# Kernel optimization log

Hardware: AMD Instinct MI355X
Metric: run time of the kernel (lower is better)

The kernel has to match this reference:

```python
import jax, jax.numpy as jnp
import numpy as np

TANH_EPS = 1e-06
LOG2PI = float(np.log(2.0 * np.pi))


def _atanh(x):
    x = jnp.clip(x, -1.0 + TANH_EPS, 1.0 - TANH_EPS)
    return 0.5 * (jnp.log1p(x) - jnp.log1p(-x))


def setup_inputs() -> dict:
    key = jax.random.key(0)
    ks = jax.random.split(key, 12)
    T, B, O, H, A = 256, 1024, 128, 128, 8
    s = 0.05
    return {
        "obs_seq": jax.random.normal(ks[0], (T, B, O), jnp.float32),
        "actions_seq": jax.random.uniform(ks[1], (T, B, A), jnp.float32, -0.99, 0.99),
        "dones_seq": (jax.random.uniform(ks[2], (T, B)) < 0.02).astype(jnp.float32),
        "h0": jnp.zeros((B, H), jnp.float32),
        "c0": jnp.zeros((B, H), jnp.float32),
        "enc_w1": s * jax.random.normal(ks[3], (H, O), jnp.float32),
        "enc_b1": jnp.zeros((H,), jnp.float32),
        "enc_w2": s * jax.random.normal(ks[4], (H, H), jnp.float32),
        "enc_b2": jnp.zeros((H,), jnp.float32),
        "w_ih": s * jax.random.normal(ks[5], (4 * H, H), jnp.float32),
        "w_hh": s * jax.random.normal(ks[6], (4 * H, H), jnp.float32),
        "b_ih": jnp.zeros((4 * H,), jnp.float32),
        "b_hh": jnp.zeros((4 * H,), jnp.float32),
        "am_w": 0.01 * jax.random.normal(ks[7], (A, H), jnp.float32),
        "am_b": jnp.zeros((A,), jnp.float32),
        "actor_logstd": jnp.zeros((A,), jnp.float32),
        "cr_w": s * jax.random.normal(ks[8], (1, H), jnp.float32),
        "cr_b": jnp.zeros((1,), jnp.float32),
    }


def reference(obs_seq, actions_seq, dones_seq, h0, c0,
              enc_w1, enc_b1, enc_w2, enc_b2,
              w_ih, w_hh, b_ih, b_hh,
              am_w, am_b, actor_logstd, cr_w, cr_b):
    # Encoder (batched over all timesteps): two tanh MLP layers.
    x = jnp.tanh(jnp.einsum('tbo,ho->tbh', obs_seq, enc_w1) + enc_b1)
    x = jnp.tanh(jnp.einsum('tbh,gh->tbg', x, enc_w2) + enc_b2)
    # Precompute input contribution to gates: [T, B, 4H]
    xg = jnp.einsum('tbh,gh->tbg', x, w_ih) + b_ih

    def step(carry, inp):
        h, c = carry
        xg_t, d_t = inp
        m = (1.0 - d_t)[:, None]  # done-masking reset
        h = h * m
        c = c * m
        g = xg_t + h @ w_hh.T + b_hh
        i, f, gg, o = jnp.split(g, 4, axis=-1)
        c2 = jax.nn.sigmoid(f) * c + jax.nn.sigmoid(i) * jnp.tanh(gg)
        h2 = jax.nn.sigmoid(o) * jnp.tanh(c2)
        return (h2, c2), h2

    (hT, cT), ys = jax.lax.scan(step, (h0, c0), (xg, dones_seq))  # ys: [T, B, H]

    values = (jnp.einsum('tbh,vh->tbv', ys, cr_w) + cr_b)[..., 0]  # [T, B]
    mean = jnp.einsum('tbh,ah->tba', ys, am_w) + am_b  # [T, B, A]
    logstd = actor_logstd  # [A]
    u = _atanh(actions_seq)
    # Normal log-prob per dim, summed over action dims
    z = (u - mean) * jnp.exp(-logstd)
    lp_gauss = jnp.sum(-0.5 * z * z - logstd - 0.5 * LOG2PI, axis=-1)
    log_jac = jnp.sum(jnp.log(1.0 - actions_seq ** 2 + TANH_EPS), axis=-1)
    logprobs = lp_gauss - log_jac
    entropies = jnp.sum(0.5 + 0.5 * LOG2PI + logstd) + log_jac
    return logprobs, entropies, values, hT, cT
```

## Files before the change

### kernel.cpp

```cpp
#include <hip/hip_runtime.h>

typedef float f32x4 __attribute__((ext_vector_type(4)));
typedef short short8 __attribute__((ext_vector_type(8)));
typedef short s16x4 __attribute__((ext_vector_type(4)));

#define MFMA16(a, b, c) __builtin_amdgcn_mfma_f32_16x16x32_bf16((a), (b), (c), 0, 0, 0)

#define T_ 256
#define B_ 1024
#define H_ 128
#define TB_ 262144
#define BH_ 131072
#define LOG2PI_F 1.8378770664093453f
#define LN2_F 0.6931471805599453f
#define LOG2E_F 1.4426950408889634f

__device__ inline short f2bf(float f) {
    unsigned u = __builtin_bit_cast(unsigned, f);
    u += 0x7fffu + ((u >> 16) & 1u);
    return (short)(u >> 16);
}
__device__ inline float fexp(float x) { return __builtin_amdgcn_exp2f(x * LOG2E_F); }
__device__ inline float fsigm(float x) { return __builtin_amdgcn_rcpf(1.f + fexp(-x)); }
__device__ inline float ftanh(float x) { return 1.f - 2.f * __builtin_amdgcn_rcpf(fexp(2.f * x) + 1.f); }

__device__ inline short8 pack8(float4 u0, float4 u1) {
    short8 p;
    p[0] = f2bf(u0.x); p[1] = f2bf(u0.y); p[2] = f2bf(u0.z); p[3] = f2bf(u0.w);
    p[4] = f2bf(u1.x); p[5] = f2bf(u1.y); p[6] = f2bf(u1.z); p[7] = f2bf(u1.w);
    return p;
}

__global__ __launch_bounds__(512, 4) void ex_kernel(
    const float* __restrict__ obs, const float* __restrict__ eb1,
    const float* __restrict__ eb2,
    const float* __restrict__ w1f, const float* __restrict__ w2f,
    short* __restrict__ x2p)
{
    __shared__ __align__(16) short xtA[64 * 128];
    __shared__ __align__(16) short xtB[64 * 128];
    __shared__ __align__(16) short xtC[64 * 128];
    const int tid = threadIdx.x;
    const int l = tid & 63, w = tid >> 6;
    const int l15 = l & 15, kg = l >> 4;
    const int srow = tid >> 3, sln = tid & 7;
    const int ssw = (srow & 7) << 3;

    short8 fw1[4], fw2[4];
#pragma unroll
    for (int kk = 0; kk < 4; ++kk) {
        const float* s1 = w1f + (w * 16 + l15) * 128 + kk * 32 + 8 * kg;
        const float* s2 = w2f + (w * 16 + l15) * 128 + kk * 32 + 8 * kg;
        fw1[kk] = pack8(*(const float4*)s1, *(const float4*)(s1 + 4));
        fw2[kk] = pack8(*(const float4*)s2, *(const float4*)(s2 + 4));
        asm volatile("" : "+v"(fw1[kk]), "+v"(fw2[kk]));
    }
    const float bb1 = eb1[w * 16 + l15], bb2 = eb2[w * 16 + l15];

    const int NT = 8;
    const int t0 = blockIdx.x * NT;

    {
        const float* src = obs + ((size_t)t0 * 64 + srow) * 128 + sln * 16;
#pragma unroll
        for (int ii = 0; ii < 2; ++ii) {
            float4 v0 = *(const float4*)(src + ii * 8);
            float4 v1 = *(const float4*)(src + ii * 8 + 4);
            *(short8*)(xtA + srow * 128 + ((sln * 16 + ii * 8) ^ ssw)) = pack8(v0, v1);
        }
    }
    __syncthreads();

    for (int i = 0; i < NT; ++i) {
        const int tile = t0 + i;
        short* bufO = (i & 1) ? xtB : xtA;
        short* bufN = (i & 1) ? xtA : xtB;

        float4 pf[4];
        {
            const int tn = (i + 1 < NT) ? tile + 1 : tile;
            const float* src = obs + ((size_t)tn * 64 + srow) * 128 + sln * 16;
#pragma unroll
            for (int ii = 0; ii < 4; ++ii) pf[ii] = *(const float4*)(src + ii * 4);
        }

#pragma unroll
        for (int mf = 0; mf < 4; ++mf) {
            const int ra = mf * 16 + l15, swa = (ra & 7) << 3;
            short8 a[4];
#pragma unroll
            for (int kk = 0; kk < 4; ++kk)
                a[kk] = *(const short8*)&bufO[ra * 128 + ((kk * 32 + 8 * kg) ^ swa)];
            f32x4 acc = {bb1, bb1, bb1, bb1};
#pragma unroll
            for (int kk = 0; kk < 4; ++kk) acc = MFMA16(a[kk], fw1[kk], acc);
#pragma unroll
            for (int j = 0; j < 4; ++j) {
                int rw = mf * 16 + kg * 4 + j;
                xtC[rw * 128 + ((w * 16 + l15) ^ ((rw & 7) << 3))] = f2bf(ftanh(acc[j]));
            }
        }
        __syncthreads();

        const int t = (tile * 64) >> 10;
        const int b_base = (tile * 64) & 1023;
#pragma unroll
        for (int mf = 0; mf < 4; ++mf) {
            const int ra = mf * 16 + l15, swa = (ra & 7) << 3;
            short8 a[4];
#pragma unroll
            for (int kk = 0; kk < 4; ++kk)
                a[kk] = *(const short8*)&xtC[ra * 128 + ((kk * 32 + 8 * kg) ^ swa)];
            f32x4 acc = {bb2, bb2, bb2, bb2};
#pragma unroll
            for (int kk = 0; kk < 4; ++kk) acc = MFMA16(a[kk], fw2[kk], acc);
#pragma unroll
            for (int j = 0; j < 4; ++j) {
                int b = b_base + mf * 16 + kg * 4 + j;
                size_t idx = (((size_t)t * 256 + (b >> 2)) * 4 + (b & 3)) * 128 + w * 16 + l15;
                x2p[idx] = f2bf(ftanh(acc[j]));
            }
        }
#pragma unroll
        for (int ii = 0; ii < 2; ++ii) {
            *(short8*)(bufN + srow * 128 + ((sln * 16 + ii * 8) ^ ssw)) =
                pack8(pf[ii * 2], pf[ii * 2 + 1]);
        }
        __syncthreads();
    }
}

__global__ __launch_bounds__(512) void lstm_kernel(
    const short* __restrict__ x2p, const float* __restrict__ whh,
    const float* __restrict__ wih,
    const float* __restrict__ h0, const float* __restrict__ c0,
    const float* __restrict__ bhh, const float* __restrict__ bih,
    const float* __restrict__ dones,
    const float* __restrict__ amw, const float* __restrict__ crw,
    const float* __restrict__ amb, const float* __restrict__ crb,
    const float* __restrict__ lstd, const float* __restrict__ actions,
    float* __restrict__ out)
{
    __shared__ __align__(16) short hbuf[2][4 * 160];
    __shared__ __align__(16) short hring[16 * 640];
    __shared__ __align__(16) short x2b[2][16 * 160];
    __shared__ float dlds[1028];
    __shared__ float hd[1024 * 12];
    const int tid = threadIdx.x;
    const int l = tid & 63, w = tid >> 6;
    const int l15 = l & 15, kg = l >> 4;
    const int b0 = blockIdx.x * 4;
    const int d = w * 16 + l15;
    const int blk = blockIdx.x;
    const int xsw = (l15 & 7) << 3;

    short8 bfr[4][4], bfi[4][4];
#pragma unroll
    for (int s = 0; s < 4; ++s)
#pragma unroll
        for (int kk = 0; kk < 4; ++kk) {
            const float* sr = whh + ((s * 128 + d) * 128 + kk * 32 + 8 * kg);
            const float* si = wih + ((s * 128 + d) * 128 + kk * 32 + 8 * kg);
            bfr[s][kk] = pack8(*(const float4*)sr, *(const float4*)(sr + 4));
            bfi[s][kk] = pack8(*(const float4*)si, *(const float4*)(si + 4));
            asm volatile("" : "+v"(bfr[s][kk]), "+v"(bfi[s][kk]));
        }

    short8 hb4[4];
#pragma unroll
    for (int kk = 0; kk < 4; ++kk) {
        if (l15 == 0) {
            const float* s0 = crw + kk * 32 + 8 * kg;
            hb4[kk] = pack8(*(const float4*)s0, *(const float4*)(s0 + 4));
        } else if (l15 <= 8) {
            const float* s0 = amw + (l15 - 1) * 128 + kk * 32 + 8 * kg;
            hb4[kk] = pack8(*(const float4*)s0, *(const float4*)(s0 + 4));
        } else {
            hb4[kk] = short8{0, 0, 0, 0, 0, 0, 0, 0};
        }
        asm volatile("" : "+v"(hb4[kk]));
    }
    const float biasH = (l15 == 0) ? crb[0] : (l15 <= 8 ? amb[l15 - 1] : 0.f);

    for (int i = tid; i < 1028; i += 512) {
        int t = i >> 2, jj = i & 3;
        dlds[i] = (t < 256) ? 1.f - dones[t * 1024 + b0 + jj] : 1.f;
    }

    float bh[4];
#pragma unroll
    for (int s = 0; s < 4; ++s) bh[s] = bhh[s * 128 + d] + bih[s * 128 + d];

    const int st_toff = tid >> 7, st_j = (tid >> 5) & 3, st_dim = (tid & 31) * 4;
    const int st_row = st_j * 4 + st_toff;
    const int xrow160 = st_row * 160 + (st_dim ^ ((st_row & 7) << 3));
#define X2GIDX(G) ((((size_t)(((G) * 4 + st_toff) <= 255 ? ((G) * 4 + st_toff) : 255) * 256 + blk) * 4 + st_j) * 128 + st_dim)

    {
        s16x4 v0 = *(const s16x4*)(x2p + X2GIDX(0));
        s16x4 v1 = *(const s16x4*)(x2p + X2GIDX(1));
        *(s16x4*)&x2b[0][xrow160] = v0;
        *(s16x4*)&x2b[1][xrow160] = v1;
    }
    s16x4 xpf = *(const s16x4*)(x2p + X2GIDX(2));
    asm volatile("s_waitcnt lgkmcnt(0)" ::: "memory");
    __syncthreads();

    f32x4 xgA[4], xgB[4];
#pragma unroll
    for (int s = 0; s < 4; ++s) {
        short8 ax[4];
#pragma unroll
        for (int kk = 0; kk < 4; ++kk)
            ax[kk] = *(const short8*)&x2b[0][l15 * 160 + ((kk * 32 + kg * 8) ^ xsw)];
        f32x4 accX = {bh[s], bh[s], bh[s], bh[s]};
#pragma unroll
        for (int kk = 0; kk < 4; ++kk) accX = MFMA16(ax[kk], bfi[s][kk], accX);
        xgA[s] = accX;
    }

    float h = h0[(b0 + kg) * 128 + d];
    float c = c0[(b0 + kg) * 128 + d];
    hbuf[0][kg * 160 + d] = f2bf(h * dlds[kg]);
    asm volatile("s_waitcnt lgkmcnt(0)" ::: "memory");
    __syncthreads();

    const int aoff = (l15 >> 2) * 160;
    float mreg = dlds[kg];

#define LSTM_STEP(t, hb, i_s, xgC, xgN, x2R, DO_T3, GNEXT, DO_HEAD)                        \
    {                                                                                      \
        short8 a[4];                                                                       \
        _Pragma("unroll")                                                                  \
        for (int kk = 0; kk < 4; ++kk)                                                     \
            a[kk] = *(const short8*)&hbuf[hb][aoff + kk * 32 + kg * 8];                    \
        f32x4 acc[4];                                                                      \
        _Pragma("unroll")                                                                  \
        for (int s = 0; s < 4; ++s) acc[s] = xgC[s];                                       \
        _Pragma("unroll")                                                                  \
        for (int kk = 0; kk < 4; ++kk)                                                     \
            _Pragma("unroll")                                                              \
            for (int s = 0; s < 4; ++s) acc[s] = MFMA16(a[kk], bfr[s][kk], acc[s]);        \
        {           \
            short8 ax[4];                                                                  \
            _Pragma("unroll")                                                              \
            for (int kk = 0; kk < 4; ++kk)                                                 \
                ax[kk] = *(const short8*)&x2R[l15 * 160 + ((kk * 32 + kg * 8) ^ xsw)];     \
            f32x4 accX = {bh[i_s], bh[i_s], bh[i_s], bh[i_s]};                             \
            _Pragma("unroll")                                                              \
            for (int kk = 0; kk < 4; ++kk) accX = MFMA16(ax[kk], bfi[i_s][kk], accX);      \
            xgN[i_s] = accX;                                                               \
        }                                                                                  \
        if (DO_HEAD) {                 \
            int th = (t) - 8 + w;                                                          \
            const short* hr = &hring[(th & 15) * 640];                                     \
            short8 ah[4];                                                                  \
            _Pragma("unroll")                                                              \
            for (int kk = 0; kk < 4; ++kk)                                                 \
                ah[kk] = *(const short8*)&hr[aoff + kk * 32 + kg * 8];                     \
            f32x4 aH = {biasH, biasH, biasH, biasH};                                       \
            _Pragma("unroll")                                                              \
            for (int kk = 0; kk < 4; ++kk) aH = MFMA16(ah[kk], hb4[kk], aH);               \
            if (l15 < 9) hd[((th) * 4 + kg) * 12 + l15] = aH[0];                           \
        }                                                                                  \
        if (DO_T3) {                                                                      \
            *(s16x4*)&x2W[xrow160] = xpf;                                                  \
            xpf = *(const s16x4*)(x2p + X2GIDX(GNEXT));                                    \
        }                                                                                  \
        float mn = dlds[((t) + 1) * 4 + kg];                                               \
        float gi = acc[0][i_s];                                                            \
        float gf = acc[1][i_s];                                                            \
        float gg = acc[2][i_s];                                                            \
        float go = acc[3][i_s];                                                            \
        c = fsigm(gf) * (c * mreg) + fsigm(gi) * ftanh(gg);                                \
        float h2 = fsigm(go) * ftanh(c);                                                   \
        h = h2;                                                                            \
        mreg = mn;                                                                         \
        hbuf[(hb) ^ 1][kg * 160 + d] = f2bf(h2 * mn);                                      \
        hring[((t) & 15) * 640 + kg * 160 + d] = f2bf(h2);                                 \
        asm volatile("s_waitcnt lgkmcnt(0)" ::: "memory");                                 \
        __builtin_amdgcn_s_barrier();                                                      \
        asm volatile("" ::: "memory");                                                     \
    }

    for (int g = 0; g < 64; g += 2) {
        {
            const int tb = g * 4;
            const short* x2R = &x2b[1][0];
            short* x2W = &x2b[0][0];
            LSTM_STEP(tb + 0, 0, 0, xgA, xgB, x2R, 0, 0, (g > 0));
            LSTM_STEP(tb + 1, 1, 1, xgA, xgB, x2R, 0, 0, 0);
            LSTM_STEP(tb + 2, 0, 2, xgA, xgB, x2R, 0, 0, 0);
            LSTM_STEP(tb + 3, 1, 3, xgA, xgB, x2R, 1, (g + 3), 0);
        }
        {
            const int tb = (g + 1) * 4;
            const short* x2R = &x2b[0][0];
            short* x2W = &x2b[1][0];
            LSTM_STEP(tb + 0, 0, 0, xgB, xgA, x2R, 0, 0, 0);
            LSTM_STEP(tb + 1, 1, 1, xgB, xgA, x2R, 0, 0, 0);
            LSTM_STEP(tb + 2, 0, 2, xgB, xgA, x2R, 0, 0, 0);
            LSTM_STEP(tb + 3, 1, 3, xgB, xgA, x2R, 1, (g + 4), 0);
        }
    }
#undef LSTM_STEP
#undef X2GIDX

    {
        int th = 248 + w;
        const short* hr = &hring[(th & 15) * 640];
        short8 ah[4];
#pragma unroll
        for (int kk = 0; kk < 4; ++kk)
            ah[kk] = *(const short8*)&hr[aoff + kk * 32 + kg * 8];
        f32x4 aH = {biasH, biasH, biasH, biasH};
#pragma unroll
        for (int kk = 0; kk < 4; ++kk) aH = MFMA16(ah[kk], hb4[kk], aH);
        if (l15 < 9) hd[(th * 4 + kg) * 12 + l15] = aH[0];
    }

    out[3 * TB_ + (b0 + kg) * 128 + d] = h;
    out[3 * TB_ + BH_ + (b0 + kg) * 128 + d] = c;

    __syncthreads();
    for (int rr = tid; rr < 1024; rr += 512) {
        const int t = rr >> 2, bb = rr & 3;
        const float* hp = &hd[rr * 12];
        const float* ap = actions + ((size_t)t * 1024 + b0 + bb) * 8;
        float4 a0 = *(const float4*)(ap);
        float4 a1 = *(const float4*)(ap + 4);
        float act[8] = {a0.x, a0.y, a0.z, a0.w, a1.x, a1.y, a1.z, a1.w};
        float lp = 0.f, lj = 0.f, entS = 0.f;
#pragma unroll
        for (int ai = 0; ai < 8; ++ai) {
            float x = act[ai];
            float xc = fminf(fmaxf(x, -1.f + 1e-6f), 1.f - 1e-6f);
            float u = 0.5f * LN2_F *
                      (__builtin_amdgcn_logf(1.f + xc) - __builtin_amdgcn_logf(1.f - xc));
            float ls = lstd[ai];
            float z = (u - hp[1 + ai]) * fexp(-ls);
            lp += -0.5f * z * z - ls;
            lj += LN2_F * __builtin_amdgcn_logf(1.f - x * x + 1e-6f);
            entS += ls;
        }
        lp -= 8.f * 0.5f * LOG2PI_F;
        entS += 8.f * (0.5f + 0.5f * LOG2PI_F);
        const int r = t * 1024 + b0 + bb;
        out[r] = lp - lj;
        out[TB_ + r] = entS + lj;
        out[2 * TB_ + r] = hp[0];
    }
}

extern "C" void kernel_launch(void* const* d_in, const int* in_sizes, int n_in,
                              void* d_out, int out_size, void* d_ws, size_t ws_size,
                              hipStream_t stream) {
    const float* obs   = (const float*)d_in[0];
    const float* acts  = (const float*)d_in[1];
    const float* dones = (const float*)d_in[2];
    const float* h0    = (const float*)d_in[3];
    const float* c0    = (const float*)d_in[4];
    const float* w1    = (const float*)d_in[5];
    const float* b1    = (const float*)d_in[6];
    const float* w2    = (const float*)d_in[7];
    const float* b2    = (const float*)d_in[8];
    const float* wih   = (const float*)d_in[9];
    const float* whh   = (const float*)d_in[10];
    const float* bih   = (const float*)d_in[11];
    const float* bhh   = (const float*)d_in[12];
    const float* amw   = (const float*)d_in[13];
    const float* amb   = (const float*)d_in[14];
    const float* lstd  = (const float*)d_in[15];
    const float* crw   = (const float*)d_in[16];
    const float* crb   = (const float*)d_in[17];
    float* out = (float*)d_out;

    short* x2p = (short*)d_ws;
    if (ws_size < (size_t)67108864) return;

    hipLaunchKernelGGL(ex_kernel, dim3(512), dim3(512), 0, stream,
                       obs, b1, b2, w1, w2, x2p);
    hipLaunchKernelGGL(lstm_kernel, dim3(256), dim3(512), 0, stream,
                       x2p, whh, wih, h0, c0, bhh, bih, dones,
                       amw, crw, amb, crb, lstd, acts, out);
}
```

Measured before the change: 212.4 us.

## Split LSTM waves into recurrent-GEMM producers and gate/input-projection consumers

Wave specialisation in the LSTM kernel: waves 0-3 hold W_hh for one gate each and compute the recurrent matmul, writing pre-activations to a shared gbuf. Waves 4-7 hold W_ih, compute the next chunk's input projection, then read gbuf to apply the cell update for two hidden dims each. The aim is to shorten the serial recurrent critical path by spreading its matmul and nonlinearities across wave groups. In exchange each step now needs two barriers and an LDS round trip, and the head projections move to the matmul waves.

```diff
diff --git a/kernel.cpp b/kernel.cpp
--- a/kernel.cpp
+++ b/kernel.cpp
@@ -29,6 +29,28 @@
     p[0] = f2bf(u0.x); p[1] = f2bf(u0.y); p[2] = f2bf(u0.z); p[3] = f2bf(u0.w);
     p[4] = f2bf(u1.x); p[5] = f2bf(u1.y); p[6] = f2bf(u1.z); p[7] = f2bf(u1.w);
     return p;
+}
+
+__device__ __forceinline__ size_t x2gidx(int G, int toff, int j, int dim, int blk) {
+    int tt = G * 4 + toff; tt = tt <= 255 ? tt : 255;
+    return (((size_t)tt * 256 + blk) * 4 + j) * 128 + dim;
+}
+
+__device__ __forceinline__ void do_head(
+    const short* hring, const f32x4* poolp, float biasH,
+    int aoff, int kg, int l15, float* hd, int th)
+{
+    const short* hr = &hring[(th & 15) * 640];
+    short8 ah0 = *(const short8*)&hr[aoff + 0 * 32 + kg * 8];
+    short8 ah1 = *(const short8*)&hr[aoff + 1 * 32 + kg * 8];
+    short8 ah2 = *(const short8*)&hr[aoff + 2 * 32 + kg * 8];
+    short8 ah3 = *(const short8*)&hr[aoff + 3 * 32 + kg * 8];
+    f32x4 aH = {biasH, biasH, biasH, biasH};
+    aH = MFMA16(ah0, __builtin_bit_cast(short8, poolp[8]), aH);
+    aH = MFMA16(ah1, __builtin_bit_cast(short8, poolp[9]), aH);
+    aH = MFMA16(ah2, __builtin_bit_cast(short8, poolp[10]), aH);
+    aH = MFMA16(ah3, __builtin_bit_cast(short8, poolp[11]), aH);
+    if (l15 < 9) hd[(th * 4 + kg) * 12 + l15] = aH[0];
 }
 
 __global__ __launch_bounds__(512, 4) void ex_kernel(
@@ -144,140 +166,206 @@
     __shared__ __align__(16) short hbuf[2][4 * 160];
     __shared__ __align__(16) short hring[16 * 640];
     __shared__ __align__(16) short x2b[2][16 * 160];
+    __shared__ __align__(16) float gbuf[2176];
     __shared__ float dlds[1028];
     __shared__ float hd[1024 * 12];
     const int tid = threadIdx.x;
     const int l = tid & 63, w = tid >> 6;
     const int l15 = l & 15, kg = l >> 4;
     const int b0 = blockIdx.x * 4;
-    const int d = w * 16 + l15;
     const int blk = blockIdx.x;
     const int xsw = (l15 & 7) << 3;
-
-    short8 bfr[4][4], bfi[4][4];
-#pragma unroll
-    for (int s = 0; s < 4; ++s)
+    const bool isG = (w < 4);
+    const int e = w & 3;
+    const int d0 = e * 32 + l15, d1 = d0 + 16;
+    const int aoff = (l15 >> 2) * 160;
+
+    short8 wB[32];
+    f32x4 pool[16];
+    float biasH = 0.f;
+    s16x4 xpfa, xpfb;
+    float c0_ = 0.f, c1_ = 0.f, h0_ = 0.f, h1_ = 0.f, mreg = 1.f;
+
+    const int sa = tid & 255;
+    const int ta_toff = sa >> 7, ta_j = (sa >> 5) & 3, ta_dim = (sa & 31) * 4;
+    const int ra_ = ta_j * 4 + ta_toff;
+    const int xrowA = ra_ * 160 + (ta_dim ^ ((ra_ & 7) << 3));
+    const int sb = (tid & 255) + 256;
+    const int tb_toff = sb >> 7, tb_j = (sb >> 5) & 3, tb_dim = (sb & 31) * 4;
+    const int rb_ = tb_j * 4 + tb_toff;
+    const int xrowB = rb_ * 160 + (tb_dim ^ ((rb_ & 7) << 3));
+
+    if (isG) {
+#pragma unroll
+        for (int ct = 0; ct < 8; ++ct)
+#pragma unroll
+            for (int kk = 0; kk < 4; ++kk) {
+                const float* s0 = whh + ((w * 128 + ct * 16 + l15) * 128 + kk * 32 + 8 * kg);
+                wB[ct * 4 + kk] = pack8(*(const float4*)s0, *(const float4*)(s0 + 4));
+            }
 #pragma unroll
         for (int kk = 0; kk < 4; ++kk) {
-            const float* sr = whh + ((s * 128 + d) * 128 + kk * 32 + 8 * kg);
-            const float* si = wih + ((s * 128 + d) * 128 + kk * 32 + 8 * kg);
-            bfr[s][kk] = pack8(*(const float4*)sr, *(const float4*)(sr + 4));
-            bfi[s][kk] = pack8(*(const float4*)si, *(const float4*)(si + 4));
-            asm volatile("" : "+v"(bfr[s][kk]), "+v"(bfi[s][kk]));
-        }
-
-    short8 hb4[4];
-#pragma unroll
-    for (int kk = 0; kk < 4; ++kk) {
-        if (l15 == 0) {
-            const float* s0 = crw + kk * 32 + 8 * kg;
-            hb4[kk] = pack8(*(const float4*)s0, *(const float4*)(s0 + 4));
-        } else if (l15 <= 8) {
-            const float* s0 = amw + (l15 - 1) * 128 + kk * 32 + 8 * kg;
-            hb4[kk] = pack8(*(const float4*)s0, *(const float4*)(s0 + 4));
-        } else {
-            hb4[kk] = short8{0, 0, 0, 0, 0, 0, 0, 0};
-        }
-        asm volatile("" : "+v"(hb4[kk]));
-    }
-    const float biasH = (l15 == 0) ? crb[0] : (l15 <= 8 ? amb[l15 - 1] : 0.f);
+            short8 hq;
+            if (l15 == 0) {
+                const float* s0 = crw + kk * 32 + 8 * kg;
+                hq = pack8(*(const float4*)s0, *(const float4*)(s0 + 4));
+            } else if (l15 <= 8) {
+                const float* s0 = amw + (l15 - 1) * 128 + kk * 32 + 8 * kg;
+                hq = pack8(*(const float4*)s0, *(const float4*)(s0 + 4));
+            } else {
+                hq = short8{0, 0, 0, 0, 0, 0, 0, 0};
+            }
+            pool[8 + kk] = __builtin_bit_cast(f32x4, hq);
+        }
+        biasH = (l15 == 0) ? crb[0] : (l15 <= 8 ? amb[l15 - 1] : 0.f);
+        f32x4 bA, bB;
+#pragma unroll
+        for (int ct = 0; ct < 4; ++ct) {
+            bA[ct] = bhh[w * 128 + ct * 16 + l15] + bih[w * 128 + ct * 16 + l15];
+            bB[ct] = bhh[w * 128 + (ct + 4) * 16 + l15] + bih[w * 128 + (ct + 4) * 16 + l15];
+        }
+        pool[12] = bA; pool[13] = bB;
+    } else {
+#pragma unroll
+        for (int s = 0; s < 4; ++s)
+#pragma unroll
+            for (int ct2 = 0; ct2 < 2; ++ct2)
+#pragma unroll
+                for (int kk = 0; kk < 4; ++kk) {
+                    const float* s0 = wih + ((s * 128 + e * 32 + ct2 * 16 + l15) * 128 + kk * 32 + 8 * kg);
+                    wB[(s * 2 + ct2) * 4 + kk] = pack8(*(const float4*)s0, *(const float4*)(s0 + 4));
+                }
+        h0_ = h0[(b0 + kg) * 128 + d0]; h1_ = h0[(b0 + kg) * 128 + d1];
+        c0_ = c0[(b0 + kg) * 128 + d0]; c1_ = c0[(b0 + kg) * 128 + d1];
+    }
+#pragma unroll
+    for (int i = 0; i < 32; ++i) asm volatile("" : "+v"(wB[i]));
 
     for (int i = tid; i < 1028; i += 512) {
         int t = i >> 2, jj = i & 3;
         dlds[i] = (t < 256) ? 1.f - dones[t * 1024 + b0 + jj] : 1.f;
     }
 
-    float bh[4];
-#pragma unroll
-    for (int s = 0; s < 4; ++s) bh[s] = bhh[s * 128 + d] + bih[s * 128 + d];
-
-    const int st_toff = tid >> 7, st_j = (tid >> 5) & 3, st_dim = (tid & 31) * 4;
-    const int st_row = st_j * 4 + st_toff;
-    const int xrow160 = st_row * 160 + (st_dim ^ ((st_row & 7) << 3));
-#define X2GIDX(G) ((((size_t)(((G) * 4 + st_toff) <= 255 ? ((G) * 4 + st_toff) : 255) * 256 + blk) * 4 + st_j) * 128 + st_dim)
-
-    {
-        s16x4 v0 = *(const s16x4*)(x2p + X2GIDX(0));
-        s16x4 v1 = *(const s16x4*)(x2p + X2GIDX(1));
-        *(s16x4*)&x2b[0][xrow160] = v0;
-        *(s16x4*)&x2b[1][xrow160] = v1;
-    }
-    s16x4 xpf = *(const s16x4*)(x2p + X2GIDX(2));
+    if (isG) {
+        s16x4 va0 = *(const s16x4*)(x2p + x2gidx(0, ta_toff, ta_j, ta_dim, blk));
+        s16x4 vb0 = *(const s16x4*)(x2p + x2gidx(0, tb_toff, tb_j, tb_dim, blk));
+        s16x4 va1 = *(const s16x4*)(x2p + x2gidx(1, ta_toff, ta_j, ta_dim, blk));
+        s16x4 vb1 = *(const s16x4*)(x2p + x2gidx(1, tb_toff, tb_j, tb_dim, blk));
+        *(s16x4*)&x2b[0][xrowA] = va0;
+        *(s16x4*)&x2b[0][xrowB] = vb0;
+        *(s16x4*)&x2b[1][xrowA] = va1;
+        *(s16x4*)&x2b[1][xrowB] = vb1;
+        xpfa = *(const s16x4*)(x2p + x2gidx(2, ta_toff, ta_j, ta_dim, blk));
+        xpfb = *(const s16x4*)(x2p + x2gidx(2, tb_toff, tb_j, tb_dim, blk));
+    }
     asm volatile("s_waitcnt lgkmcnt(0)" ::: "memory");
     __syncthreads();
 
-    f32x4 xgA[4], xgB[4];
-#pragma unroll
-    for (int s = 0; s < 4; ++s) {
+    if (!isG) {
         short8 ax[4];
 #pragma unroll
         for (int kk = 0; kk < 4; ++kk)
             ax[kk] = *(const short8*)&x2b[0][l15 * 160 + ((kk * 32 + kg * 8) ^ xsw)];
-        f32x4 accX = {bh[s], bh[s], bh[s], bh[s]};
-#pragma unroll
-        for (int kk = 0; kk < 4; ++kk) accX = MFMA16(ax[kk], bfi[s][kk], accX);
-        xgA[s] = accX;
-    }
-
-    float h = h0[(b0 + kg) * 128 + d];
-    float c = c0[(b0 + kg) * 128 + d];
-    hbuf[0][kg * 160 + d] = f2bf(h * dlds[kg]);
+#pragma unroll
+        for (int s = 0; s < 4; ++s)
+#pragma unroll
+            for (int ct2 = 0; ct2 < 2; ++ct2) {
+                f32x4 accX = {0.f, 0.f, 0.f, 0.f};
+#pragma unroll
+                for (int kk = 0; kk < 4; ++kk)
+                    accX = MFMA16(ax[kk], wB[(s * 2 + ct2) * 4 + kk], accX);
+                pool[s * 2 + ct2] = accX;
+            }
+        mreg = dlds[kg];
+        hbuf[0][kg * 160 + d0] = f2bf(h0_ * mreg);
+        hbuf[0][kg * 160 + d1] = f2bf(h1_ * mreg);
+    }
     asm volatile("s_waitcnt lgkmcnt(0)" ::: "memory");
     __syncthreads();
 
-    const int aoff = (l15 >> 2) * 160;
-    float mreg = dlds[kg];
-
-#define LSTM_STEP(t, hb, i_s, xgC, xgN, x2R, DO_T3, GNEXT, DO_HEAD)                        \
+#define STEP(t, hb, i_s, XGC, XGN, x2R, x2W, DO_T3, GNEXT, DO_HEAD)                        \
     {                                                                                      \
-        short8 a[4];                                                                       \
-        _Pragma("unroll")                                                                  \
-        for (int kk = 0; kk < 4; ++kk)                                                     \
-            a[kk] = *(const short8*)&hbuf[hb][aoff + kk * 32 + kg * 8];                    \
-        f32x4 acc[4];                                                                      \
-        _Pragma("unroll")                                                                  \
-        for (int s = 0; s < 4; ++s) acc[s] = xgC[s];                                       \
-        _Pragma("unroll")                                                                  \
-        for (int kk = 0; kk < 4; ++kk)                                                     \
-            _Pragma("unroll")                                                              \
-            for (int s = 0; s < 4; ++s) acc[s] = MFMA16(a[kk], bfr[s][kk], acc[s]);        \
-        {           \
+        if (isG) {                                                                         \
+            short8 a[4];                                                                   \
+            _Pragma("unroll")                                                              \
+            for (int kk = 0; kk < 4; ++kk)                                                 \
+                a[kk] = *(const short8*)&hbuf[hb][aoff + kk * 32 + kg * 8];                \
+            f32x4 acc[4];                                                                  \
+            _Pragma("unroll")                                                              \
+            for (int ct = 0; ct < 4; ++ct) {                                               \
+                float bv = pool[12][ct];                                                   \
+                f32x4 ini = {bv, bv, bv, bv};                                              \
+                acc[ct] = ini;                                                             \
+            }                                                                              \
+            _Pragma("unroll")                                                              \
+            for (int kk = 0; kk < 4; ++kk)                                                 \
+                _Pragma("unroll")                                                          \
+                for (int ct = 0; ct < 4; ++ct)                                             \
+                    acc[ct] = MFMA16(a[kk], wB[ct * 4 + kk], acc[ct]);                     \
+            _Pragma("unroll")                                                              \
+            for (int ct = 0; ct < 4; ++ct)                                                 \
+                gbuf[(w * 4 + kg) * 136 + ct * 16 + l15] = acc[ct][0];                     \
+            _Pragma("unroll")                                                              \
+            for (int ct = 0; ct < 4; ++ct) {                                               \
+                float bv = pool[13][ct];                                                   \
+                f32x4 ini = {bv, bv, bv, bv};                                              \
+                acc[ct] = ini;                                                             \
+            }                                                                              \
+            _Pragma("unroll")                                                              \
+            for (int kk = 0; kk < 4; ++kk)                                                 \
+                _Pragma("unroll")                                                          \
+                for (int ct = 0; ct < 4; ++ct)                                             \
+                    acc[ct] = MFMA16(a[kk], wB[(ct + 4) * 4 + kk], acc[ct]);               \
+            _Pragma("unroll")                                                              \
+            for (int ct = 0; ct < 4; ++ct)                                                 \
+                gbuf[(w * 4 + kg) * 136 + (ct + 4) * 16 + l15] = acc[ct][0];               \
+            if (DO_T3) {                                                                   \
+                *(s16x4*)&x2W[xrowA] = xpfa;                                               \
+                *(s16x4*)&x2W[xrowB] = xpfb;                                               \
+                xpfa = *(const s16x4*)(x2p + x2gidx(GNEXT, ta_toff, ta_j, ta_dim, blk));   \
+                xpfb = *(const s16x4*)(x2p + x2gidx(GNEXT, tb_toff, tb_j, tb_dim, blk));   \
+            }                                                                              \
+        } else {                                                                           \
             short8 ax[4];                                                                  \
             _Pragma("unroll")                                                              \
             for (int kk = 0; kk < 4; ++kk)                                                 \
                 ax[kk] = *(const short8*)&x2R[l15 * 160 + ((kk * 32 + kg * 8) ^ xsw)];     \
-            f32x4 accX = {bh[i_s], bh[i_s], bh[i_s], bh[i_s]};                             \
-            _Pragma("unroll")                                                              \
-            for (int kk = 0; kk < 4; ++kk) accX = MFMA16(ax[kk], bfi[i_s][kk], accX);      \
-            xgN[i_s] = accX;                                                               \
+            f32x4 xt0 = {0.f, 0.f, 0.f, 0.f};                                              \
+            f32x4 xt1 = {0.f, 0.f, 0.f, 0.f};                                              \
+            _Pragma("unroll")                                                              \
+            for (int kk = 0; kk < 4; ++kk) {                                               \
+                xt0 = MFMA16(ax[kk], wB[((i_s) * 2 + 0) * 4 + kk], xt0);                   \
+                xt1 = MFMA16(ax[kk], wB[((i_s) * 2 + 1) * 4 + kk], xt1);                   \
+            }                                                                              \
+            pool[(XGN) + (i_s) * 2 + 0] = xt0;                                             \
+            pool[(XGN) + (i_s) * 2 + 1] = xt1;                                             \
         }                                                                                  \
-        if (DO_HEAD) {                 \
-            int th = (t) - 8 + w;                                                          \
-            const short* hr = &hring[(th & 15) * 640];                                     \
-            short8 ah[4];                                                                  \
-            _Pragma("unroll")                                                              \
-            for (int kk = 0; kk < 4; ++kk)                                                 \
-                ah[kk] = *(const short8*)&hr[aoff + kk * 32 + kg * 8];                     \
-            f32x4 aH = {biasH, biasH, biasH, biasH};                                       \
-            _Pragma("unroll")                                                              \
-            for (int kk = 0; kk < 4; ++kk) aH = MFMA16(ah[kk], hb4[kk], aH);               \
-            if (l15 < 9) hd[((th) * 4 + kg) * 12 + l15] = aH[0];                           \
+        asm volatile("s_waitcnt lgkmcnt(0)" ::: "memory");                                 \
+        __builtin_amdgcn_s_barrier();                                                      \
+        asm volatile("" ::: "memory");                                                     \
+        if (!isG) {                                                                        \
+            float mn = dlds[((t) + 1) * 4 + kg];                                           \
+            float gi0 = gbuf[(0 * 4 + kg) * 136 + d0] + pool[(XGC) + 0][i_s];              \
+            float gf0 = gbuf[(1 * 4 + kg) * 136 + d0] + pool[(XGC) + 2][i_s];              \
+            float gg0 = gbuf[(2 * 4 + kg) * 136 + d0] + pool[(XGC) + 4][i_s];              \
+            float go0 = gbuf[(3 * 4 + kg) * 136 + d0] + pool[(XGC) + 6][i_s];              \
+            float gi1 = gbuf[(0 * 4 + kg) * 136 + d1] + pool[(XGC) + 1][i_s];              \
+            float gf1 = gbuf[(1 * 4 + kg) * 136 + d1] + pool[(XGC) + 3][i_s];              \
+            float gg1 = gbuf[(2 * 4 + kg) * 136 + d1] + pool[(XGC) + 5][i_s];              \
+            float go1 = gbuf[(3 * 4 + kg) * 136 + d1] + pool[(XGC) + 7][i_s];              \
+            c0_ = fsigm(gf0) * (c0_ * mreg) + fsigm(gi0) * ftanh(gg0);                     \
+            float h20 = fsigm(go0) * ftanh(c0_);                                           \
+            c1_ = fsigm(gf1) * (c1_ * mreg) + fsigm(gi1) * ftanh(gg1);                     \
+            float h21 = fsigm(go1) * ftanh(c1_);                                           \
+            hbuf[(hb) ^ 1][kg * 160 + d0] = f2bf(h20 * mn);                                \
+            hbuf[(hb) ^ 1][kg * 160 + d1] = f2bf(h21 * mn);                                \
+            hring[((t) & 15) * 640 + kg * 160 + d0] = f2bf(h20);                           \
+            hring[((t) & 15) * 640 + kg * 160 + d1] = f2bf(h21);                           \
+            h0_ = h20; h1_ = h21; mreg = mn;                                               \
+        } else if (DO_HEAD) {                                                              \
+            do_head(hring, pool, biasH, aoff, kg, l15, hd, (t) - 8 + w * 2);               \
+            do_head(hring, pool, biasH, aoff, kg, l15, hd, (t) - 8 + w * 2 + 1);           \
         }                                                                                  \
-        if (DO_T3) {                                                                      \
-            *(s16x4*)&x2W[xrow160] = xpf;                                                  \
-            xpf = *(const s16x4*)(x2p + X2GIDX(GNEXT));                                    \
-        }                                                                                  \
-        float mn = dlds[((t) + 1) * 4 + kg];                                               \
-        float gi = acc[0][i_s];                                                            \
-        float gf = acc[1][i_s];                                                            \
-        float gg = acc[2][i_s];                                                            \
-        float go = acc[3][i_s];                                                            \
-        c = fsigm(gf) * (c * mreg) + fsigm(gi) * ftanh(gg);                                \
-        float h2 = fsigm(go) * ftanh(c);                                                   \
-        h = h2;                                                                            \
-        mreg = mn;                                                                         \
-        hbuf[(hb) ^ 1][kg * 160 + d] = f2bf(h2 * mn);                                      \
-        hring[((t) & 15) * 640 + kg * 160 + d] = f2bf(h2);                                 \
         asm volatile("s_waitcnt lgkmcnt(0)" ::: "memory");                                 \
         __builtin_amdgcn_s_barrier();                                                      \
         asm volatile("" ::: "memory");                                                     \
@@ -288,39 +376,32 @@
             const int tb = g * 4;
             const short* x2R = &x2b[1][0];
             short* x2W = &x2b[0][0];
-            LSTM_STEP(tb + 0, 0, 0, xgA, xgB, x2R, 0, 0, (g > 0));
-            LSTM_STEP(tb + 1, 1, 1, xgA, xgB, x2R, 0, 0, 0);
-            LSTM_STEP(tb + 2, 0, 2, xgA, xgB, x2R, 0, 0, 0);
-            LSTM_STEP(tb + 3, 1, 3, xgA, xgB, x2R, 1, (g + 3), 0);
+            STEP(tb + 0, 0, 0, 0, 8, x2R, x2W, 0, 0, (g > 0));
+            STEP(tb + 1, 1, 1, 0, 8, x2R, x2W, 0, 0, 0);
+            STEP(tb + 2, 0, 2, 0, 8, x2R, x2W, 0, 0, 0);
+            STEP(tb + 3, 1, 3, 0, 8, x2R, x2W, 1, (g + 3), 0);
         }
         {
             const int tb = (g + 1) * 4;
             const short* x2R = &x2b[0][0];
             short* x2W = &x2b[1][0];
-            LSTM_STEP(tb + 0, 0, 0, xgB, xgA, x2R, 0, 0, 0);
-            LSTM_STEP(tb + 1, 1, 1, xgB, xgA, x2R, 0, 0, 0);
-            LSTM_STEP(tb + 2, 0, 2, xgB, xgA, x2R, 0, 0, 0);
-            LSTM_STEP(tb + 3, 1, 3, xgB, xgA, x2R, 1, (g + 4), 0);
-        }
-    }
-#undef LSTM_STEP
-#undef X2GIDX
-
-    {
-        int th = 248 + w;
-        const short* hr = &hring[(th & 15) * 640];
-        short8 ah[4];
-#pragma unroll
-        for (int kk = 0; kk < 4; ++kk)
-            ah[kk] = *(const short8*)&hr[aoff + kk * 32 + kg * 8];
-        f32x4 aH = {biasH, biasH, biasH, biasH};
-#pragma unroll
-        for (int kk = 0; kk < 4; ++kk) aH = MFMA16(ah[kk], hb4[kk], aH);
-        if (l15 < 9) hd[(th * 4 + kg) * 12 + l15] = aH[0];
-    }
-
-    out[3 * TB_ + (b0 + kg) * 128 + d] = h;
-    out[3 * TB_ + BH_ + (b0 + kg) * 128 + d] = c;
+            STEP(tb + 0, 0, 0, 8, 0, x2R, x2W, 0, 0, 0);
+            STEP(tb + 1, 1, 1, 8, 0, x2R, x2W, 0, 0, 0);
+            STEP(tb + 2, 0, 2, 8, 0, x2R, x2W, 0, 0, 0);
+            STEP(tb + 3, 1, 3, 8, 0, x2R, x2W, 1, (g + 4), 0);
+        }
+    }
+#undef STEP
+
+    if (isG) {
+        do_head(hring, pool, biasH, aoff, kg, l15, hd, 248 + w * 2);
+        do_head(hring, pool, biasH, aoff, kg, l15, hd, 248 + w * 2 + 1);
+    } else {
+        out[3 * TB_ + (b0 + kg) * 128 + d0] = h0_;
+        out[3 * TB_ + (b0 + kg) * 128 + d1] = h1_;
+        out[3 * TB_ + BH_ + (b0 + kg) * 128 + d0] = c0_;
+        out[3 * TB_ + BH_ + (b0 + kg) * 128 + d1] = c1_;
+    }
 
     __syncthreads();
     for (int rr = tid; rr < 1024; rr += 512) {
```

Result: slower. 363.9 us (+71.3%).
